# Performance work log

Measured on AMD Instinct MI355X. Metric: run time of the kernel, lower is better.

The kernel has to match this reference:

```python
import jax, jax.numpy as jnp
import numpy as np

KS = 7                 # sconv_kernel_size
PAD = (KS - 1) // 2
SIMS_SCALE = 10.0      # sims_norm_scale
EPS = 1e-5


def setup_inputs() -> dict:
    key = jax.random.key(0)
    k1, k2, k3, k4 = jax.random.split(key, 4)
    T, C, H, W = 4, 3, 192, 192
    S = 300
    x = jax.random.normal(k1, (T, C, H, W), jnp.float32)
    spix = jax.random.randint(k2, (T, H, W), 0, S, dtype=jnp.int32)
    W_lin = jax.random.normal(k3, (C, C * KS * KS), jnp.float32) * 0.05
    b_lin = jax.random.normal(k4, (C,), jnp.float32) * 0.05
    return {"x": x, "spix": spix, "W_lin": W_lin, "b_lin": b_lin, "n_spix": S}


def _get_sims(x, spix, n_spix, scale):
    # x: [T,C,H,W], spix: [T,H,W] with contiguous ids in [0, n_spix)
    T, C, H, W = x.shape
    feats = x.transpose(0, 2, 3, 1).reshape(T, H * W, C)   # t (h w) f
    ids = spix.reshape(T, H * W)

    def pool(f, i):
        s = jax.ops.segment_sum(f, i, num_segments=n_spix)                      # [S,C]
        c = jax.ops.segment_sum(jnp.ones((f.shape[0],), f.dtype), i, num_segments=n_spix)  # [S]
        return s / jnp.maximum(c, 1.0)[:, None], c

    means, cnt = jax.vmap(pool)(feats, ids)                # [T,S,C], [T,S]
    # squared euclidean distance (cdist ** 2)
    d2 = (jnp.sum(feats * feats, -1)[:, :, None]
          + jnp.sum(means * means, -1)[:, None, :]
          - 2.0 * jnp.einsum('tnc,tsc->tns', feats, means))
    d2 = jnp.maximum(d2, 0.0)                              # [T,HW,S]
    # superpixels absent from frame t get distance inf (pwd[mask] = inf)
    d2 = jnp.where((cnt > 0)[:, None, :], d2, jnp.inf)
    sims = jax.nn.softmax(-scale * d2, axis=-1)            # softmax over superpixels
    return sims.reshape(T, H, W, n_spix)                   # [T,H,W,S]


def _prod_attn(sims):
    # non-local 'prod' search, zero flow, ws=KS: dot product of sims vectors
    # between each pixel and its KSxKS neighborhood (zero-padded borders)
    T, H, W, S = sims.shape
    p = jnp.pad(sims, ((0, 0), (PAD, PAD), (PAD, PAD), (0, 0)))
    attn = [jnp.einsum('thws,thws->thw', sims, p[:, dy:dy + H, dx:dx + W, :])
            for dy in range(KS) for dx in range(KS)]
    return jnp.stack(attn, -1)                             # [T,H,W,KS*KS]


def _unfold(x):
    # torch.nn.Unfold(kernel_size=KS, padding=PAD): zero pad, row-major window
    T, C, H, W = x.shape
    p = jnp.pad(x, ((0, 0), (0, 0), (PAD, PAD), (PAD, PAD)))
    pats = [p[:, :, dy:dy + H, dx:dx + W] for dy in range(KS) for dx in range(KS)]
    return jnp.stack(pats, 2)                              # [T,C,KS*KS,H,W]


def reference(x, spix, W_lin, b_lin, n_spix):
    T, C, H, W = x.shape
    sims = _get_sims(x, spix, n_spix, SIMS_SCALE)          # [T,H,W,S]
    rw = _prod_attn(sims)                                  # [T,H,W,K2]
    # apply_norm('max'): divide by max over neighborhood
    rw = rw / (EPS + jnp.max(rw, axis=-1, keepdims=True))
    Wk = W_lin.reshape(W_lin.shape[0], C, KS * KS)         # [od,id,k2]
    pats = _unfold(x)                                      # [T,id,k2,H,W]
    # out[t,o,h,w] = sum_{i,k} W[o,i,k] * rw[t,h,w,k] * patch[t,i,k,h,w] + b[o]
    out = jnp.einsum('oik,thwk,tikhw->tohw', Wk, rw, pats) + b_lin[None, :, None, None]
    return out
```

## Files before the change

### kernel.cpp

```cpp
#include <hip/hip_runtime.h>
#include <math.h>

#define TT 4
#define HH 192
#define WW 192
#define SS 300
#define SP 320
#define HW (HH*WW)
#define PD 3
#define HSZ 22
#define NHP 484
#define NG 1936
#define LOG2E 1.44269504088896340736f
#define MOFF 16384
#define ZOFF (MOFF + TT*HW)

typedef _Float16 h8 __attribute__((ext_vector_type(8)));
typedef float f4 __attribute__((ext_vector_type(4)));


__global__ void k_zero(float* ws) {
    int i = blockIdx.x * 256 + threadIdx.x;
    if (i < TT * SS * 4) ws[i] = 0.f;
}

__launch_bounds__(256)
__global__ void k_accum(const float* __restrict__ x, const int* __restrict__ spix,
                        float* __restrict__ ws) {
    __shared__ float ls[SS * 4];
    const int tid = threadIdx.x;
    const int t = blockIdx.y, seg = blockIdx.x;
    for (int i = tid; i < SS * 4; i += 256) ls[i] = 0.f;
    __syncthreads();
#pragma unroll
    for (int it = 0; it < 9; it++) {
        int px = seg * 2304 + it * 256 + tid;
        int s = spix[t * HW + px];
        atomicAdd(&ls[s * 4 + 0], x[(t * 3 + 0) * HW + px]);
        atomicAdd(&ls[s * 4 + 1], x[(t * 3 + 1) * HW + px]);
        atomicAdd(&ls[s * 4 + 2], x[(t * 3 + 2) * HW + px]);
        atomicAdd(&ls[s * 4 + 3], 1.f);
    }
    __syncthreads();
    for (int i = tid; i < SS * 4; i += 256) {
        float v = ls[i];
        if (v != 0.f) {
            int s = i >> 2, c = i & 3;
            if (c < 3) atomicAdd(&ws[(t * SS + s) * 3 + c], v);
            else       atomicAdd(&ws[3600 + t * SS + s], v);
        }
    }
}

__global__ void k_means(float* __restrict__ ws) {
    int i = blockIdx.x * 256 + threadIdx.x;
    if (i >= TT * SP) return;
    int t = i / SP, s = i - t * SP;
    const float* sums = ws;
    const float* cnts = ws + TT * SS * 3;
    float4* m4 = (float4*)(ws + 4800);
    float4 m;
    if (s < SS) {
        float c = cnts[t * SS + s];
        float inv = 1.f / fmaxf(c, 1.f);
        float mx = sums[(t * SS + s) * 3 + 0] * inv;
        float my = sums[(t * SS + s) * 3 + 1] * inv;
        float mz = sums[(t * SS + s) * 3 + 2] * inv;
        m.x = 20.f * LOG2E * mx; m.y = 20.f * LOG2E * my; m.z = 20.f * LOG2E * mz;
        m.w = (c > 0.f) ? (-10.f * LOG2E * (mx * mx + my * my + mz * mz)) : -INFINITY;
    } else {
        m.x = 0.f; m.y = 0.f; m.z = 0.f; m.w = -INFINITY;
    }
    m4[t * SP + s] = m;
}

__launch_bounds__(256)
__global__ void k_prep(const float* __restrict__ x, float* __restrict__ ws) {
    __shared__ float4 sm[SP];
    const int tid = threadIdx.x;
    const int t = blockIdx.y;
    const int p = blockIdx.x * 256 + tid;
    const float4* m4 = (const float4*)(ws + 4800) + t * SP;
    for (int i = tid; i < SP; i += 256) sm[i] = m4[i];
    __syncthreads();
    const float fx = x[(t * 3 + 0) * HW + p];
    const float fy = x[(t * 3 + 1) * HW + p];
    const float fz = x[(t * 3 + 2) * HW + p];

    float M0 = -INFINITY, M1 = -INFINITY;
#pragma unroll 4
    for (int s = 0; s < SP; s += 2) {
        float4 a = sm[s], b = sm[s + 1];
        M0 = fmaxf(M0, fmaf(fx, a.x, fmaf(fy, a.y, fmaf(fz, a.z, a.w))));
        M1 = fmaxf(M1, fmaf(fx, b.x, fmaf(fy, b.y, fmaf(fz, b.z, b.w))));
    }
    const float M = fmaxf(M0, M1);
    float Z0 = 0.f, Z1 = 0.f;
#pragma unroll 4
    for (int s = 0; s < SP; s += 2) {
        float4 a = sm[s], b = sm[s + 1];
        Z0 += exp2f(fmaf(fx, a.x, fmaf(fy, a.y, fmaf(fz, a.z, a.w))) - M);
        Z1 += exp2f(fmaf(fx, b.x, fmaf(fy, b.y, fmaf(fz, b.z, b.w))) - M);
    }
    ws[MOFF + t * HW + p] = M;
    ws[ZOFF + t * HW + p] = 1.f / (Z0 + Z1);
}

#define REP49(M) M(0)M(1)M(2)M(3)M(4)M(5)M(6)M(7)M(8)M(9)M(10)M(11)M(12)M(13) \
    M(14)M(15)M(16)M(17)M(18)M(19)M(20)M(21)M(22)M(23)M(24)M(25)M(26)M(27) \
    M(28)M(29)M(30)M(31)M(32)M(33)M(34)M(35)M(36)M(37)M(38)M(39)M(40)M(41) \
    M(42)M(43)M(44)M(45)M(46)M(47)M(48)

#define QOFF(k) (((k) / 7 - PD) * HSZ + ((k) % 7 - PD))


__launch_bounds__(512, 2)
__global__ void k_main(const float* __restrict__ x, const float* __restrict__ Wlin,
                       const float* __restrict__ blin, const float* __restrict__ ws,
                       float* __restrict__ out) {
    __shared__ __align__(16) char ebuf[2][NG * 16];
    __shared__ float4 sfh[NHP];
    __shared__ float  sW[441];

    const int tid = threadIdx.x;
    const int wid = tid >> 6, lane = tid & 63;
    const int pxc = lane & 15, kg = lane >> 4;
    const int t = blockIdx.z;
    const int gx0 = blockIdx.x * 16 - PD, gy0 = blockIdx.y * 16 - PD;
    const float4* m4 = (const float4*)(ws + 4800) + t * SP;

    for (int i = tid; i < 441; i += 512) sW[i] = Wlin[i];

    float fx = 0.f, fy = 0.f, fz = 0.f, M = INFINITY;
    if (tid < NHP) {
        int hy = tid / HSZ, hx = tid - hy * HSZ;
        int gy = gy0 + hy, gx = gx0 + hx;
        float iZ = 0.f;
        if (gy >= 0 && gy < HH && gx >= 0 && gx < WW) {
            int p = gy * WW + gx;
            fx = x[(t * 3 + 0) * HW + p];
            fy = x[(t * 3 + 1) * HW + p];
            fz = x[(t * 3 + 2) * HW + p];
            M  = ws[MOFF + t * HW + p];
            iZ = ws[ZOFF + t * HW + p];
        }
        sfh[tid] = make_float4(fx, fy, fz, iZ);
    }

#define PHASEB(cc, bb) if (tid < NHP) { \
        char* dst = ebuf[bb]; \
        _Pragma("unroll") \
        for (int jd = 0; jd < 4; jd++) { \
            h8 v; \
            _Pragma("unroll") \
            for (int e = 0; e < 4; e++) { \
                float4 ma = m4[(cc) * 32 + jd * 8 + 2 * e]; \
                float4 mb = m4[(cc) * 32 + jd * 8 + 2 * e + 1]; \
                float E0 = exp2f(fmaf(fx, ma.x, fmaf(fy, ma.y, fmaf(fz, ma.z, ma.w))) - M); \
                float E1 = exp2f(fmaf(fx, mb.x, fmaf(fy, mb.y, fmaf(fz, mb.z, mb.w))) - M); \
                auto pr = __builtin_amdgcn_cvt_pkrtz(E0, E1); \
                v[2 * e] = (_Float16)pr.x; v[2 * e + 1] = (_Float16)pr.y; \
            } \
            *(h8*)(dst + (jd * NHP + tid) * 16) = v; \
        } }

    const int r0 = 2 * wid;
    const int gA0 = kg * NHP + (r0 + PD) * HSZ + PD + pxc;
    const int gA1 = gA0 + HSZ;
    const int bcol2 = (16 + pxc > 21) ? 21 : 16 + pxc;
    const int gB1 = kg * NHP + r0 * HSZ + pxc;
    const int gB2 = kg * NHP + r0 * HSZ + bcol2;

    f4 zero4 = {0.f, 0.f, 0.f, 0.f};
    f4 aP[7], aQ[7], aR[7], aS[7];
#pragma unroll
    for (int d = 0; d < 7; d++) { aP[d] = zero4; aQ[d] = zero4; aR[d] = zero4; aS[d] = zero4; }

    PHASEB(0, 0)

#pragma unroll 1
    for (int c = 0; c < 10; c++) {
        __syncthreads();
        if (c < 9) { PHASEB(c + 1, (c + 1) & 1) }
        const char* pb = ebuf[c & 1];
        h8 A0 = *(const h8*)(pb + gA0 * 16);
        h8 A1 = *(const h8*)(pb + gA1 * 16);
        h8 b1 = *(const h8*)(pb + gB1 * 16);
        h8 b2 = *(const h8*)(pb + gB2 * 16);
        aP[0] = __builtin_amdgcn_mfma_f32_16x16x32_f16(A0, b1, aP[0], 0, 0, 0);
        aQ[0] = __builtin_amdgcn_mfma_f32_16x16x32_f16(A0, b2, aQ[0], 0, 0, 0);
#pragma unroll
        for (int d = 1; d < 7; d++) {
            h8 n1 = *(const h8*)(pb + (gB1 + d * HSZ) * 16);
            h8 n2 = *(const h8*)(pb + (gB2 + d * HSZ) * 16);
            aP[d]     = __builtin_amdgcn_mfma_f32_16x16x32_f16(A0, n1, aP[d], 0, 0, 0);
            aR[d - 1] = __builtin_amdgcn_mfma_f32_16x16x32_f16(A1, n1, aR[d - 1], 0, 0, 0);
            aQ[d]     = __builtin_amdgcn_mfma_f32_16x16x32_f16(A0, n2, aQ[d], 0, 0, 0);
            aS[d - 1] = __builtin_amdgcn_mfma_f32_16x16x32_f16(A1, n2, aS[d - 1], 0, 0, 0);
        }
        h8 l1 = *(const h8*)(pb + (gB1 + 7 * HSZ) * 16);
        h8 l2 = *(const h8*)(pb + (gB2 + 7 * HSZ) * 16);
        aR[6] = __builtin_amdgcn_mfma_f32_16x16x32_f16(A1, l1, aR[6], 0, 0, 0);
        aS[6] = __builtin_amdgcn_mfma_f32_16x16x32_f16(A1, l2, aS[6], 0, 0, 0);
    }
    __syncthreads();

    float* attn = (float*)ebuf;
#pragma unroll
    for (int d = 0; d < 7; d++) {
#pragma unroll
        for (int reg = 0; reg < 4; reg++) {
            int i = 4 * kg + reg;
            int u1 = pxc - i;
            int u2 = u1 + 16;
            if ((unsigned)u1 <= 6u) {
                attn[(r0 * 16 + i) * 51 + d * 7 + u1] = aP[d][reg];
                attn[((r0 + 1) * 16 + i) * 51 + d * 7 + u1] = aR[d][reg];
            }
            if ((unsigned)u2 <= 6u) {
                attn[(r0 * 16 + i) * 51 + d * 7 + u2] = aQ[d][reg];
                attn[((r0 + 1) * 16 + i) * 51 + d * 7 + u2] = aS[d][reg];
            }
        }
    }
    __syncthreads();

    if (tid < 256) {
        const int r = tid >> 4, cq = tid & 15;
        const int own = (r + PD) * HSZ + (cq + PD);
        const float* ap = attn + tid * 51;
        float mx = 0.f;
#define PK1(k) mx = fmaxf(mx, ap[k] * sfh[own + QOFF(k)].w);
        REP49(PK1)
#undef PK1
        const float iZp = sfh[own].w;
        const float inv = 1.f / (1e-5f / iZp + mx);

        float o0 = blin[0], o1 = blin[1], o2 = blin[2];
#define PK2(k) { float4 f = sfh[own + QOFF(k)]; \
        float rwk = ap[k] * f.w * inv; \
        o0 += rwk * (sW[k] * f.x + sW[49 + (k)] * f.y + sW[98 + (k)] * f.z); \
        o1 += rwk * (sW[147 + (k)] * f.x + sW[196 + (k)] * f.y + sW[245 + (k)] * f.z); \
        o2 += rwk * (sW[294 + (k)] * f.x + sW[343 + (k)] * f.y + sW[392 + (k)] * f.z); }
        REP49(PK2)
#undef PK2

        int p = (gy0 + PD + r) * WW + gx0 + PD + cq;
        out[(t * 3 + 0) * HW + p] = o0;
        out[(t * 3 + 1) * HW + p] = o1;
        out[(t * 3 + 2) * HW + p] = o2;
    }
}

extern "C" void kernel_launch(void* const* d_in, const int* in_sizes, int n_in,
                              void* d_out, int out_size, void* d_ws, size_t ws_size,
                              hipStream_t stream) {
    (void)in_sizes; (void)n_in; (void)out_size; (void)ws_size;
    const float* x    = (const float*)d_in[0];
    const int*   spix = (const int*)d_in[1];
    const float* Wlin = (const float*)d_in[2];
    const float* blin = (const float*)d_in[3];
    float* out = (float*)d_out;
    float* ws  = (float*)d_ws;

    hipLaunchKernelGGL(k_zero,  dim3(19), dim3(256), 0, stream, ws);
    hipLaunchKernelGGL(k_accum, dim3(16, TT), dim3(256), 0, stream, x, spix, ws);
    hipLaunchKernelGGL(k_means, dim3((TT * SP + 255) / 256), dim3(256), 0, stream, ws);
    hipLaunchKernelGGL(k_prep,  dim3(HW / 256, TT), dim3(256), 0, stream, x, ws);
    hipLaunchKernelGGL(k_main,  dim3(WW / 16, HH / 16, TT), dim3(512), 0, stream,
                       x, Wlin, blin, ws, out);
}
```

Baseline: 132.4 us.

## Double k_main block to 1024 threads and process two pixels per thread in k_prep

k_main now launches 1024 threads per block. Each wave handles one output row instead of two, and the fp16 exp-table generation is split across two halves of the thread block, so each thread computes two of the four 8-wide chunks. This cuts per-thread MFMA accumulators and exp work, aiming for more parallelism and less register pressure, but it may cost occupancy given the large LDS footprint and the 1024-thread launch bound. k_prep processes two pixels per thread so the shared means table is reused across both, halving the grid.

```diff
diff --git a/kernel.cpp b/kernel.cpp
--- a/kernel.cpp
+++ b/kernel.cpp
@@ -79,31 +79,32 @@
     __shared__ float4 sm[SP];
     const int tid = threadIdx.x;
     const int t = blockIdx.y;
-    const int p = blockIdx.x * 256 + tid;
+    const int p0 = blockIdx.x * 512 + tid;
+    const int p1 = p0 + 256;
     const float4* m4 = (const float4*)(ws + 4800) + t * SP;
     for (int i = tid; i < SP; i += 256) sm[i] = m4[i];
     __syncthreads();
-    const float fx = x[(t * 3 + 0) * HW + p];
-    const float fy = x[(t * 3 + 1) * HW + p];
-    const float fz = x[(t * 3 + 2) * HW + p];
+    const float f0x = x[(t * 3 + 0) * HW + p0], f0y = x[(t * 3 + 1) * HW + p0], f0z = x[(t * 3 + 2) * HW + p0];
+    const float f1x = x[(t * 3 + 0) * HW + p1], f1y = x[(t * 3 + 1) * HW + p1], f1z = x[(t * 3 + 2) * HW + p1];
 
     float M0 = -INFINITY, M1 = -INFINITY;
 #pragma unroll 4
-    for (int s = 0; s < SP; s += 2) {
-        float4 a = sm[s], b = sm[s + 1];
-        M0 = fmaxf(M0, fmaf(fx, a.x, fmaf(fy, a.y, fmaf(fz, a.z, a.w))));
-        M1 = fmaxf(M1, fmaf(fx, b.x, fmaf(fy, b.y, fmaf(fz, b.z, b.w))));
-    }
-    const float M = fmaxf(M0, M1);
+    for (int s = 0; s < SP; s++) {
+        float4 a = sm[s];
+        M0 = fmaxf(M0, fmaf(f0x, a.x, fmaf(f0y, a.y, fmaf(f0z, a.z, a.w))));
+        M1 = fmaxf(M1, fmaf(f1x, a.x, fmaf(f1y, a.y, fmaf(f1z, a.z, a.w))));
+    }
     float Z0 = 0.f, Z1 = 0.f;
 #pragma unroll 4
-    for (int s = 0; s < SP; s += 2) {
-        float4 a = sm[s], b = sm[s + 1];
-        Z0 += exp2f(fmaf(fx, a.x, fmaf(fy, a.y, fmaf(fz, a.z, a.w))) - M);
-        Z1 += exp2f(fmaf(fx, b.x, fmaf(fy, b.y, fmaf(fz, b.z, b.w))) - M);
-    }
-    ws[MOFF + t * HW + p] = M;
-    ws[ZOFF + t * HW + p] = 1.f / (Z0 + Z1);
+    for (int s = 0; s < SP; s++) {
+        float4 a = sm[s];
+        Z0 += exp2f(fmaf(f0x, a.x, fmaf(f0y, a.y, fmaf(f0z, a.z, a.w))) - M0);
+        Z1 += exp2f(fmaf(f1x, a.x, fmaf(f1y, a.y, fmaf(f1z, a.z, a.w))) - M1);
+    }
+    ws[MOFF + t * HW + p0] = M0;
+    ws[MOFF + t * HW + p1] = M1;
+    ws[ZOFF + t * HW + p0] = 1.f / Z0;
+    ws[ZOFF + t * HW + p1] = 1.f / Z1;
 }
 
 #define REP49(M) M(0)M(1)M(2)M(3)M(4)M(5)M(6)M(7)M(8)M(9)M(10)M(11)M(12)M(13) \
@@ -114,7 +115,7 @@
 #define QOFF(k) (((k) / 7 - PD) * HSZ + ((k) % 7 - PD))
 
 
-__launch_bounds__(512, 2)
+__launch_bounds__(1024, 4)
 __global__ void k_main(const float* __restrict__ x, const float* __restrict__ Wlin,
                        const float* __restrict__ blin, const float* __restrict__ ws,
                        float* __restrict__ out) {
@@ -129,28 +130,31 @@
     const int gx0 = blockIdx.x * 16 - PD, gy0 = blockIdx.y * 16 - PD;
     const float4* m4 = (const float4*)(ws + 4800) + t * SP;
 
-    for (int i = tid; i < 441; i += 512) sW[i] = Wlin[i];
-
+    for (int i = tid; i < 441; i += 1024) sW[i] = Wlin[i];
+
+    const int half = (tid >= NHP) ? 1 : 0;
+    const int hp = tid - half * NHP;
     float fx = 0.f, fy = 0.f, fz = 0.f, M = INFINITY;
-    if (tid < NHP) {
-        int hy = tid / HSZ, hx = tid - hy * HSZ;
+    if (tid < 2 * NHP) {
+        int hy = hp / HSZ, hx = hp - hy * HSZ;
         int gy = gy0 + hy, gx = gx0 + hx;
-        float iZ = 0.f;
         if (gy >= 0 && gy < HH && gx >= 0 && gx < WW) {
             int p = gy * WW + gx;
             fx = x[(t * 3 + 0) * HW + p];
             fy = x[(t * 3 + 1) * HW + p];
             fz = x[(t * 3 + 2) * HW + p];
             M  = ws[MOFF + t * HW + p];
-            iZ = ws[ZOFF + t * HW + p];
-        }
-        sfh[tid] = make_float4(fx, fy, fz, iZ);
-    }
-
-#define PHASEB(cc, bb) if (tid < NHP) { \
+            if (half == 0) sfh[hp] = make_float4(fx, fy, fz, ws[ZOFF + t * HW + p]);
+        } else if (half == 0) {
+            sfh[hp] = make_float4(0.f, 0.f, 0.f, 0.f);
+        }
+    }
+
+#define PHASEB(cc, bb) if (tid < 2 * NHP) { \
         char* dst = ebuf[bb]; \
         _Pragma("unroll") \
-        for (int jd = 0; jd < 4; jd++) { \
+        for (int j2 = 0; j2 < 2; j2++) { \
+            int jd = 2 * half + j2; \
             h8 v; \
             _Pragma("unroll") \
             for (int e = 0; e < 4; e++) { \
@@ -161,20 +165,19 @@
                 auto pr = __builtin_amdgcn_cvt_pkrtz(E0, E1); \
                 v[2 * e] = (_Float16)pr.x; v[2 * e + 1] = (_Float16)pr.y; \
             } \
-            *(h8*)(dst + (jd * NHP + tid) * 16) = v; \
+            *(h8*)(dst + (jd * NHP + hp) * 16) = v; \
         } }
 
-    const int r0 = 2 * wid;
-    const int gA0 = kg * NHP + (r0 + PD) * HSZ + PD + pxc;
-    const int gA1 = gA0 + HSZ;
+    const int r = wid;
+    const int gA0 = kg * NHP + (r + PD) * HSZ + PD + pxc;
     const int bcol2 = (16 + pxc > 21) ? 21 : 16 + pxc;
-    const int gB1 = kg * NHP + r0 * HSZ + pxc;
-    const int gB2 = kg * NHP + r0 * HSZ + bcol2;
+    const int gB1 = kg * NHP + r * HSZ + pxc;
+    const int gB2 = kg * NHP + r * HSZ + bcol2;
 
     f4 zero4 = {0.f, 0.f, 0.f, 0.f};
-    f4 aP[7], aQ[7], aR[7], aS[7];
-#pragma unroll
-    for (int d = 0; d < 7; d++) { aP[d] = zero4; aQ[d] = zero4; aR[d] = zero4; aS[d] = zero4; }
+    f4 aP[7], aQ[7];
+#pragma unroll
+    for (int d = 0; d < 7; d++) { aP[d] = zero4; aQ[d] = zero4; }
 
     PHASEB(0, 0)
 
@@ -184,24 +187,13 @@
         if (c < 9) { PHASEB(c + 1, (c + 1) & 1) }
         const char* pb = ebuf[c & 1];
         h8 A0 = *(const h8*)(pb + gA0 * 16);
-        h8 A1 = *(const h8*)(pb + gA1 * 16);
-        h8 b1 = *(const h8*)(pb + gB1 * 16);
-        h8 b2 = *(const h8*)(pb + gB2 * 16);
-        aP[0] = __builtin_amdgcn_mfma_f32_16x16x32_f16(A0, b1, aP[0], 0, 0, 0);
-        aQ[0] = __builtin_amdgcn_mfma_f32_16x16x32_f16(A0, b2, aQ[0], 0, 0, 0);
-#pragma unroll
-        for (int d = 1; d < 7; d++) {
+#pragma unroll
+        for (int d = 0; d < 7; d++) {
             h8 n1 = *(const h8*)(pb + (gB1 + d * HSZ) * 16);
             h8 n2 = *(const h8*)(pb + (gB2 + d * HSZ) * 16);
-            aP[d]     = __builtin_amdgcn_mfma_f32_16x16x32_f16(A0, n1, aP[d], 0, 0, 0);
-            aR[d - 1] = __builtin_amdgcn_mfma_f32_16x16x32_f16(A1, n1, aR[d - 1], 0, 0, 0);
-            aQ[d]     = __builtin_amdgcn_mfma_f32_16x16x32_f16(A0, n2, aQ[d], 0, 0, 0);
-            aS[d - 1] = __builtin_amdgcn_mfma_f32_16x16x32_f16(A1, n2, aS[d - 1], 0, 0, 0);
-        }
-        h8 l1 = *(const h8*)(pb + (gB1 + 7 * HSZ) * 16);
-        h8 l2 = *(const h8*)(pb + (gB2 + 7 * HSZ) * 16);
-        aR[6] = __builtin_amdgcn_mfma_f32_16x16x32_f16(A1, l1, aR[6], 0, 0, 0);
-        aS[6] = __builtin_amdgcn_mfma_f32_16x16x32_f16(A1, l2, aS[6], 0, 0, 0);
+            aP[d] = __builtin_amdgcn_mfma_f32_16x16x32_f16(A0, n1, aP[d], 0, 0, 0);
+            aQ[d] = __builtin_amdgcn_mfma_f32_16x16x32_f16(A0, n2, aQ[d], 0, 0, 0);
+        }
     }
     __syncthreads();
 
@@ -213,21 +205,15 @@
             int i = 4 * kg + reg;
             int u1 = pxc - i;
             int u2 = u1 + 16;
-            if ((unsigned)u1 <= 6u) {
-                attn[(r0 * 16 + i) * 51 + d * 7 + u1] = aP[d][reg];
-                attn[((r0 + 1) * 16 + i) * 51 + d * 7 + u1] = aR[d][reg];
-            }
-            if ((unsigned)u2 <= 6u) {
-                attn[(r0 * 16 + i) * 51 + d * 7 + u2] = aQ[d][reg];
-                attn[((r0 + 1) * 16 + i) * 51 + d * 7 + u2] = aS[d][reg];
-            }
+            if ((unsigned)u1 <= 6u) attn[(r * 16 + i) * 51 + d * 7 + u1] = aP[d][reg];
+            if ((unsigned)u2 <= 6u) attn[(r * 16 + i) * 51 + d * 7 + u2] = aQ[d][reg];
         }
     }
     __syncthreads();
 
     if (tid < 256) {
-        const int r = tid >> 4, cq = tid & 15;
-        const int own = (r + PD) * HSZ + (cq + PD);
+        const int rr = tid >> 4, cq = tid & 15;
+        const int own = (rr + PD) * HSZ + (cq + PD);
         const float* ap = attn + tid * 51;
         float mx = 0.f;
 #define PK1(k) mx = fmaxf(mx, ap[k] * sfh[own + QOFF(k)].w);
@@ -245,7 +231,7 @@
         REP49(PK2)
 #undef PK2
 
-        int p = (gy0 + PD + r) * WW + gx0 + PD + cq;
+        int p = (gy0 + PD + rr) * WW + gx0 + PD + cq;
         out[(t * 3 + 0) * HW + p] = o0;
         out[(t * 3 + 1) * HW + p] = o1;
         out[(t * 3 + 2) * HW + p] = o2;
@@ -266,7 +252,7 @@
     hipLaunchKernelGGL(k_zero,  dim3(19), dim3(256), 0, stream, ws);
     hipLaunchKernelGGL(k_accum, dim3(16, TT), dim3(256), 0, stream, x, spix, ws);
     hipLaunchKernelGGL(k_means, dim3((TT * SP + 255) / 256), dim3(256), 0, stream, ws);
-    hipLaunchKernelGGL(k_prep,  dim3(HW / 256, TT), dim3(256), 0, stream, x, ws);
-    hipLaunchKernelGGL(k_main,  dim3(WW / 16, HH / 16, TT), dim3(512), 0, stream,
+    hipLaunchKernelGGL(k_prep,  dim3(HW / 512, TT), dim3(256), 0, stream, x, ws);
+    hipLaunchKernelGGL(k_main,  dim3(WW / 16, HH / 16, TT), dim3(1024), 0, stream,
                        x, Wlin, blin, ws, out);
 }
```

Measured after the change: 202.4 us. +52.8%, slower.
